# Kernel optimization log

Hardware: AMD Instinct MI355X
Metric: run time of the kernel (lower is better)

The kernel has to match this reference:

```python
import jax, jax.numpy as jnp
import numpy as np

B, S, D, M, E, K = 4, 1024, 2048, 512, 8, 2
AUX_W = 0.01


def setup_inputs() -> dict:
    key = jax.random.key(0)
    ks = jax.random.split(key, 9)
    n = lambda k, sh, fan: jax.random.normal(k, sh, jnp.float32) * (fan ** -0.5)
    return {
        "hidden_states": jax.random.normal(ks[0], (B, S, D), jnp.float32),
        "w_router": n(ks[1], (D, E), D),
        "wi0": n(ks[2], (E, D, M), D),
        "wi1": n(ks[3], (E, D, M), D),
        "wo": n(ks[4], (E, M, D), M),
        "sw_wi0": n(ks[5], (D, M), D),
        "sw_wi1": n(ks[6], (D, M), D),
        "sw_wo": n(ks[7], (M, D), M),
        "w_shared_gate": n(ks[8], (D, 1), D),
        "deterministic": 1,
    }


def reference(hidden_states, w_router, wi0, wi1, wo, sw_wi0, sw_wi1, sw_wo, w_shared_gate, deterministic):
    b, s, d = hidden_states.shape
    x = hidden_states.reshape(-1, d)  # [T, D]
    T = x.shape[0]

    # --- router: softmax over experts, top-k, renormalize top-k weights ---
    logits = (x @ w_router).astype(jnp.float32)           # [T, E]
    probs = jax.nn.softmax(logits, axis=-1)
    top_w, top_i = jax.lax.top_k(probs, K)                # [T, K]
    top_w = top_w / jnp.sum(top_w, axis=-1, keepdims=True)
    one_hot = jax.nn.one_hot(top_i, E, dtype=probs.dtype)  # [T, K, E]
    combine = jnp.einsum("tk,tke->te", top_w, one_hot)     # [T, E] sparse combine weights

    # --- load-balance aux loss (MaxText style) ---
    density = jnp.mean(jnp.sum(one_hot, axis=1), axis=0)    # fraction routed per expert
    density_proxy = jnp.mean(probs, axis=0)                 # mean router prob per expert
    load_balance_loss = jnp.mean(density * density_proxy) * (E * E) * AUX_W

    # --- routed experts: scan over experts, gated MLP, weighted combine ---
    def expert_step(acc, packed):
        wi0_e, wi1_e, wo_e, w_e = packed  # [D,M],[D,M],[M,D],[T]
        h = jax.nn.silu(x @ wi0_e) * (x @ wi1_e)            # [T, M]
        return acc + w_e[:, None] * (h @ wo_e), None

    routed, _ = jax.lax.scan(
        expert_step, jnp.zeros_like(x), (wi0, wi1, wo, combine.T)
    )

    # --- shared expert (gated MLP) + sigmoid shared gate ---
    hs = jax.nn.silu(x @ sw_wi0) * (x @ sw_wi1)
    shared = hs @ sw_wo                                     # [T, D]
    gate = jax.nn.sigmoid(x @ w_shared_gate)                # [T, 1]

    out = (routed + gate * shared).reshape(b, s, d)
    return out, load_balance_loss
```

## Files before the change

### kernel.cpp

```cpp
#include <hip/hip_runtime.h>
#include <hip/hip_bf16.h>
#include <math.h>

#define TT 4096
#define DD 2048
#define MM 512
#define EE 8

typedef __attribute__((ext_vector_type(8))) short short8;
typedef __attribute__((ext_vector_type(4))) float f32x4;

#define BARRIER() asm volatile("s_barrier" ::: "memory")

__device__ __forceinline__ unsigned short f2bf(float f) {
  union { float f; unsigned u; } v; v.f = f;
  unsigned u = v.u;
  unsigned r = u + 0x7FFFu + ((u >> 16) & 1u);
  return (unsigned short)(r >> 16);
}

__device__ __forceinline__ float bf2f(unsigned short u) {
  union { unsigned u; float f; } v; v.u = ((unsigned)u) << 16;
  return v.f;
}

__device__ __forceinline__ int imin(int a, int b) { return a < b ? a : b; }

__device__ __forceinline__ void gld16(const void* g, void* l) {
  __builtin_amdgcn_global_load_lds(
      (const __attribute__((address_space(1))) void*)g,
      (__attribute__((address_space(3))) void*)l, 16, 0, 0);
}

__global__ __launch_bounds__(256) void transpose_kernel(
    const float* __restrict__ wi0, const float* __restrict__ wi1,
    const float* __restrict__ wo, const float* __restrict__ swi0,
    const float* __restrict__ swi1, const float* __restrict__ swo,
    unsigned short* __restrict__ wi0T, unsigned short* __restrict__ wi1T,
    unsigned short* __restrict__ woT, unsigned short* __restrict__ swi0T,
    unsigned short* __restrict__ swi1T, unsigned short* __restrict__ swoT)
{
  int b = blockIdx.x;
  int tid = threadIdx.x;
  int slice = b >> 6, q = b & 63;
  const float* s; unsigned short* d;
  int R, C, tcb;
  if (slice < 8)       { s = wi0 + (size_t)slice * DD * MM;        d = wi0T + (size_t)slice * DD * MM;        R = DD; C = MM; tcb = 3; }
  else if (slice < 16) { s = wi1 + (size_t)(slice - 8) * DD * MM;  d = wi1T + (size_t)(slice - 8) * DD * MM;  R = DD; C = MM; tcb = 3; }
  else if (slice < 24) { s = wo + (size_t)(slice - 16) * MM * DD;  d = woT + (size_t)(slice - 16) * MM * DD;  R = MM; C = DD; tcb = 5; }
  else if (slice == 24){ s = swi0; d = swi0T; R = DD; C = MM; tcb = 3; }
  else if (slice == 25){ s = swi1; d = swi1T; R = DD; C = MM; tcb = 3; }
  else                 { s = swo;  d = swoT;  R = MM; C = DD; tcb = 5; }
  int ncmask = (1 << tcb) - 1;

  int wv = tid >> 6, lane = tid & 63;
  int t = q * 4 + wv;
  int c0 = (t & ncmask) * 64, r0 = (t >> tcb) * 64;
  int r8 = (lane >> 3) * 8;
  int c8 = (lane & 7) * 8;

  const float* sp = s + (size_t)(r0 + r8) * C + (c0 + c8);
  float4 v[8][2];
#pragma unroll
  for (int j = 0; j < 8; ++j) {
    v[j][0] = *(const float4*)&sp[(size_t)j * C];
    v[j][1] = *(const float4*)&sp[(size_t)j * C + 4];
  }
  __builtin_amdgcn_sched_barrier(0);
  unsigned short u[8][8];
#pragma unroll
  for (int j = 0; j < 8; ++j) {
    u[j][0] = f2bf(v[j][0].x); u[j][1] = f2bf(v[j][0].y);
    u[j][2] = f2bf(v[j][0].z); u[j][3] = f2bf(v[j][0].w);
    u[j][4] = f2bf(v[j][1].x); u[j][5] = f2bf(v[j][1].y);
    u[j][6] = f2bf(v[j][1].z); u[j][7] = f2bf(v[j][1].w);
  }
  unsigned short* dp = d + (size_t)(c0 + c8) * R + (r0 + r8);
#pragma unroll
  for (int c = 0; c < 8; ++c) {
    short8 o;
#pragma unroll
    for (int j = 0; j < 8; ++j) o[j] = (short)u[j][c];
    *(short8*)&dp[(size_t)c * R] = o;
  }
}

__global__ __launch_bounds__(256) void router_kernel(
    const float* __restrict__ x, const float* __restrict__ wr,
    const float* __restrict__ wg, unsigned short* __restrict__ xb,
    int* __restrict__ topk_i, float* __restrict__ topk_w,
    float* __restrict__ gate, int* __restrict__ cnt, float* __restrict__ proxy)
{
  __shared__ float s_proxy[EE];
  __shared__ int s_cnt[EE];
  int rb = blockIdx.x;
  int tid = threadIdx.x;
  if (tid < EE) { s_proxy[tid] = 0.f; s_cnt[tid] = 0; }
  __syncthreads();
  int wave = tid >> 6, lane = tid & 63;
  int t = rb * 4 + wave;
  const float* xr = x + (size_t)t * DD;
  unsigned short* xbr = xb + (size_t)t * DD;

  float xv[32], wgv[32];
#pragma unroll
  for (int i = 0; i < 32; ++i) xv[i] = xr[lane + i * 64];
#pragma unroll
  for (int i = 0; i < 32; ++i) wgv[i] = wg[lane + i * 64];
#pragma unroll
  for (int i = 0; i < 32; ++i) xbr[lane + i * 64] = f2bf(xv[i]);

  float p[EE];
#pragma unroll
  for (int e = 0; e < EE; ++e) p[e] = 0.f;
  float pg = 0.f;
  for (int i = 0; i < DD / 64; ++i) {
    int d = lane + i * 64;
    const float* w = wr + d * EE;
#pragma unroll
    for (int e = 0; e < EE; ++e) p[e] = fmaf(xv[i], w[e], p[e]);
    pg = fmaf(xv[i], wgv[i], pg);
  }
#pragma unroll
  for (int e = 0; e < EE; ++e) {
#pragma unroll
    for (int off = 32; off; off >>= 1) p[e] += __shfl_xor(p[e], off);
  }
#pragma unroll
  for (int off = 32; off; off >>= 1) pg += __shfl_xor(pg, off);

  if (lane == 0) {
    float mx = p[0];
#pragma unroll
    for (int e = 1; e < EE; ++e) mx = fmaxf(mx, p[e]);
    float pr[EE]; float s = 0.f;
#pragma unroll
    for (int e = 0; e < EE; ++e) { pr[e] = __expf(p[e] - mx); s += pr[e]; }
    float inv = 1.f / s;
#pragma unroll
    for (int e = 0; e < EE; ++e) pr[e] *= inv;
    int i0 = 0;
#pragma unroll
    for (int e = 1; e < EE; ++e) if (p[e] > p[i0]) i0 = e;
    int i1 = (i0 == 0) ? 1 : 0;
#pragma unroll
    for (int e = 0; e < EE; ++e) if (e != i0 && p[e] > p[i1]) i1 = e;
    float w0 = pr[i0], w1 = pr[i1], s2 = w0 + w1;
    topk_i[t * 2] = i0; topk_i[t * 2 + 1] = i1;
    topk_w[t * 2] = w0 / s2; topk_w[t * 2 + 1] = w1 / s2;
    gate[t] = 1.f / (1.f + __expf(-pg));
    atomicAdd(&s_cnt[i0], 1);
    atomicAdd(&s_cnt[i1], 1);
#pragma unroll
    for (int e = 0; e < EE; ++e) atomicAdd(&s_proxy[e], pr[e]);
  }
  __syncthreads();
  if (tid < EE) {
    atomicAdd(&cnt[tid], s_cnt[tid]);
    atomicAdd(&proxy[tid], s_proxy[tid]);
  }
}

__global__ void offsets_loss_kernel(const int* __restrict__ cnt, int* __restrict__ offs,
                                    const float* __restrict__ proxy, float* __restrict__ out_loss)
{
  if (threadIdx.x == 0 && blockIdx.x == 0) {
    int acc = 0; float l = 0.f;
    for (int e = 0; e < EE; ++e) {
      offs[e] = acc; acc += cnt[e];
      l += (float)cnt[e] * proxy[e];
    }
    out_loss[0] = l * (0.01f * (float)EE) / ((float)TT * (float)TT);
  }
}

__global__ void fill_kernel(const int* __restrict__ topk_i,
                            const int* __restrict__ offs, int* __restrict__ fillc,
                            int* __restrict__ btok, int* __restrict__ slotOf)
{
  int idx = blockIdx.x * blockDim.x + threadIdx.x;
  if (idx >= TT * 2) return;
  int e = topk_i[idx];
  int slot = atomicAdd(&fillc[e], 1);
  int p = offs[e] + slot;
  btok[p] = idx >> 1;
  slotOf[idx] = p;
}

__global__ __launch_bounds__(256) void gemm1_kernel(
    const unsigned short* __restrict__ xb,
    const unsigned short* __restrict__ wi0T, const unsigned short* __restrict__ wi1T,
    const unsigned short* __restrict__ swi0T, const unsigned short* __restrict__ swi1T,
    unsigned short* __restrict__ H, unsigned short* __restrict__ Hs,
    const int* __restrict__ btok, const int* __restrict__ cnt, const int* __restrict__ offs)
{
  __shared__ __align__(16) unsigned short lA0[128 * 64];
  __shared__ __align__(16) unsigned short lA1[128 * 64];
  __shared__ __align__(16) unsigned short lB0[128 * 64];
  __shared__ __align__(16) unsigned short lB1[128 * 64];
  int z = blockIdx.z;
  const unsigned short *w0, *w1;
  const int* tok = nullptr;
  unsigned short* Ho;
  int n;
  if (z < EE) {
    n = cnt[z];
    int rb = offs[z];
    tok = btok + rb;
    w0 = wi0T + (size_t)z * (DD * MM);
    w1 = wi1T + (size_t)z * (DD * MM);
    Ho = H + (size_t)rb * MM;
  } else { n = TT; w0 = swi0T; w1 = swi1T; Ho = Hs; }
  int row0 = blockIdx.y * 128;
  if (row0 >= n) return;
  int m0 = blockIdx.x * 64;
  int tid = threadIdx.x, lane = tid & 63, wv = tid >> 6;

  int lsub = lane >> 3;
  int chl = (lane & 7) ^ lsub;

  const unsigned short* gA[4];
  const unsigned short* gB[4];
#pragma unroll
  for (int c = 0; c < 4; ++c) {
    int row = c * 32 + wv * 8 + lsub;
    int tr;
    if (tok) tr = tok[imin(row0 + row, n - 1)];
    else     tr = row0 + row;
    gA[c] = xb + (size_t)tr * DD + chl * 8;
    int mat = row >> 6, col = row & 63;
    const unsigned short* wsel = mat ? w1 : w0;
    gB[c] = wsel + (size_t)(m0 + col) * DD + chl * 8;
  }

  int rw = (wv & 1) * 64;
  int cg = (wv >> 1) * 32;
  int fr = lane & 15;
  int grp = lane >> 4;
  int lr4 = (lane >> 4) * 4, lc = lane & 15;

  f32x4 acc[4][4];
  f32x4 zf = {0.f, 0.f, 0.f, 0.f};
#pragma unroll
  for (int i = 0; i < 4; ++i)
#pragma unroll
    for (int c = 0; c < 4; ++c) acc[i][c] = zf;

  auto stage = [&](int kk, unsigned short* la, unsigned short* lb) {
#pragma unroll
    for (int c = 0; c < 4; ++c) gld16(gA[c] + kk, la + c * 2048 + wv * 512);
#pragma unroll
    for (int c = 0; c < 4; ++c) gld16(gB[c] + kk, lb + c * 2048 + wv * 512);
  };
  auto compute = [&](const unsigned short* la, const unsigned short* lb) {
#pragma unroll
    for (int s = 0; s < 2; ++s) {
      int cq = s * 4 + grp;
      short8 af[4], bf[4];
#pragma unroll
      for (int i = 0; i < 4; ++i) {
        int row = rw + i * 16 + fr;
        af[i] = *(const short8*)&la[row * 64 + ((cq ^ (row & 7)) * 8)];
      }
#pragma unroll
      for (int c = 0; c < 4; ++c) {
        int rowb = (c >> 1) * 64 + cg + (c & 1) * 16 + fr;
        bf[c] = *(const short8*)&lb[rowb * 64 + ((cq ^ (rowb & 7)) * 8)];
      }
#pragma unroll
      for (int i = 0; i < 4; ++i)
#pragma unroll
        for (int c = 0; c < 4; ++c)
          acc[i][c] = __builtin_amdgcn_mfma_f32_16x16x32_bf16(af[i], bf[c], acc[i][c], 0, 0, 0);
    }
  };

  stage(0, lA0, lB0);
  stage(64, lA1, lB1);
  asm volatile("s_waitcnt vmcnt(8)" ::: "memory");
  BARRIER();

#pragma unroll 1
  for (int j = 0; j < DD / 128 - 1; ++j) {
    int k0 = j * 128;
    compute(lA0, lB0);
    BARRIER();
    stage(k0 + 128, lA0, lB0);
    asm volatile("s_waitcnt vmcnt(8)" ::: "memory");
    BARRIER();
    compute(lA1, lB1);
    BARRIER();
    stage(k0 + 192, lA1, lB1);
    asm volatile("s_waitcnt vmcnt(8)" ::: "memory");
    BARRIER();
  }
  compute(lA0, lB0);
  asm volatile("s_waitcnt vmcnt(0)" ::: "memory");
  BARRIER();
  compute(lA1, lB1);

#pragma unroll
  for (int i = 0; i < 4; ++i) {
#pragma unroll
    for (int c = 0; c < 2; ++c) {
#pragma unroll
      for (int rg = 0; rg < 4; ++rg) {
        int row = row0 + rw + i * 16 + lr4 + rg;
        if (row < n) {
          float a0 = acc[i][c][rg];
          float a1 = acc[i][c + 2][rg];
          float h = a0 / (1.f + __expf(-a0)) * a1;
          Ho[(size_t)row * MM + m0 + cg + c * 16 + lc] = f2bf(h);
        }
      }
    }
  }
}

__global__ __launch_bounds__(256) void gemm2_kernel(
    const unsigned short* __restrict__ H, const unsigned short* __restrict__ Hs,
    const unsigned short* __restrict__ woT, const unsigned short* __restrict__ swoT,
    unsigned short* __restrict__ Yr, unsigned short* __restrict__ Ys,
    const int* __restrict__ cnt, const int* __restrict__ offs)
{
  __shared__ __align__(16) unsigned short lA0[128 * 64];
  __shared__ __align__(16) unsigned short lA1[128 * 64];
  __shared__ __align__(16) unsigned short lB0[128 * 64];
  __shared__ __align__(16) unsigned short lB1[128 * 64];
  int z = blockIdx.z;
  int n, rb;
  const unsigned short *Hb, *wb;
  unsigned short* Yd;
  if (z < EE) { n = cnt[z]; rb = offs[z]; Hb = H + (size_t)rb * MM; wb = woT + (size_t)z * (DD * MM); Yd = Yr + (size_t)rb * DD; }
  else        { n = TT; rb = 0; Hb = Hs; wb = swoT; Yd = Ys; }
  int row0 = blockIdx.y * 128;
  if (row0 >= n) return;
  int d0 = blockIdx.x * 128;
  int tid = threadIdx.x, lane = tid & 63, wv = tid >> 6;

  int lsub = lane >> 3;
  int chl = (lane & 7) ^ lsub;

  const unsigned short* gA[4];
  const unsigned short* gB[4];
#pragma unroll
  for (int c = 0; c < 4; ++c) {
    int row = c * 32 + wv * 8 + lsub;
    int sr = imin(row0 + row, n - 1);
    gA[c] = Hb + (size_t)sr * MM + chl * 8;
    gB[c] = wb + (size_t)(d0 + row) * MM + chl * 8;
  }

  int rw = (wv & 1) * 64;
  int cw = (wv >> 1) * 64;
  int fr = lane & 15;
  int grp = lane >> 4;
  int lr4 = (lane >> 4) * 4, lc = lane & 15;

  f32x4 acc[4][4];
  f32x4 zf = {0.f, 0.f, 0.f, 0.f};
#pragma unroll
  for (int i = 0; i < 4; ++i)
#pragma unroll
    for (int c = 0; c < 4; ++c) acc[i][c] = zf;

  auto stage = [&](int kk, unsigned short* la, unsigned short* lb) {
#pragma unroll
    for (int c = 0; c < 4; ++c) gld16(gA[c] + kk, la + c * 2048 + wv * 512);
#pragma unroll
    for (int c = 0; c < 4; ++c) gld16(gB[c] + kk, lb + c * 2048 + wv * 512);
  };
  auto compute = [&](const unsigned short* la, const unsigned short* lb) {
#pragma unroll
    for (int s = 0; s < 2; ++s) {
      int cq = s * 4 + grp;
      short8 af[4], bf[4];
#pragma unroll
      for (int i = 0; i < 4; ++i) {
        int row = rw + i * 16 + fr;
        af[i] = *(const short8*)&la[row * 64 + ((cq ^ (row & 7)) * 8)];
      }
#pragma unroll
      for (int c = 0; c < 4; ++c) {
        int rowb = cw + c * 16 + fr;
        bf[c] = *(const short8*)&lb[rowb * 64 + ((cq ^ (rowb & 7)) * 8)];
      }
#pragma unroll
      for (int i = 0; i < 4; ++i)
#pragma unroll
        for (int c = 0; c < 4; ++c)
          acc[i][c] = __builtin_amdgcn_mfma_f32_16x16x32_bf16(af[i], bf[c], acc[i][c], 0, 0, 0);
    }
  };

  stage(0, lA0, lB0);
  stage(64, lA1, lB1);
  asm volatile("s_waitcnt vmcnt(8)" ::: "memory");
  BARRIER();

#pragma unroll 1
  for (int j = 0; j < MM / 128 - 1; ++j) {
    int k0 = j * 128;
    compute(lA0, lB0);
    BARRIER();
    stage(k0 + 128, lA0, lB0);
    asm volatile("s_waitcnt vmcnt(8)" ::: "memory");
    BARRIER();
    compute(lA1, lB1);
    BARRIER();
    stage(k0 + 192, lA1, lB1);
    asm volatile("s_waitcnt vmcnt(8)" ::: "memory");
    BARRIER();
  }
  compute(lA0, lB0);
  asm volatile("s_waitcnt vmcnt(0)" ::: "memory");
  BARRIER();
  compute(lA1, lB1);

#pragma unroll
  for (int i = 0; i < 4; ++i) {
#pragma unroll
    for (int c = 0; c < 4; ++c) {
#pragma unroll
      for (int rg = 0; rg < 4; ++rg) {
        int row = row0 + rw + i * 16 + lr4 + rg;
        if (row < n)
          Yd[(size_t)row * DD + d0 + cw + c * 16 + lc] = f2bf(acc[i][c][rg]);
      }
    }
  }
}

__global__ __launch_bounds__(256) void combine_kernel(
    const unsigned short* __restrict__ Yr, const unsigned short* __restrict__ Ys,
    const int* __restrict__ slotOf, const float* __restrict__ topk_w,
    const float* __restrict__ gate, float* __restrict__ out)
{
  int t = blockIdx.x;
  int d0 = threadIdx.x * 8;
  int p0 = slotOf[t * 2], p1 = slotOf[t * 2 + 1];
  float w0 = topk_w[t * 2], w1 = topk_w[t * 2 + 1], g = gate[t];
  short8 a = *(const short8*)&Yr[(size_t)p0 * DD + d0];
  short8 b = *(const short8*)&Yr[(size_t)p1 * DD + d0];
  short8 s = *(const short8*)&Ys[(size_t)t * DD + d0];
  float r[8];
#pragma unroll
  for (int j = 0; j < 8; ++j)
    r[j] = w0 * bf2f((unsigned short)a[j]) + w1 * bf2f((unsigned short)b[j])
         + g * bf2f((unsigned short)s[j]);
  float4 o0 = {r[0], r[1], r[2], r[3]};
  float4 o1 = {r[4], r[5], r[6], r[7]};
  float* op = out + (size_t)t * DD + d0;
  *(float4*)op = o0;
  *(float4*)(op + 4) = o1;
}

extern "C" void kernel_launch(void* const* d_in, const int* in_sizes, int n_in,
                              void* d_out, int out_size, void* d_ws, size_t ws_size,
                              hipStream_t stream) {
  const float* x    = (const float*)d_in[0];
  const float* wr   = (const float*)d_in[1];
  const float* wi0  = (const float*)d_in[2];
  const float* wi1  = (const float*)d_in[3];
  const float* wo   = (const float*)d_in[4];
  const float* swi0 = (const float*)d_in[5];
  const float* swi1 = (const float*)d_in[6];
  const float* swo  = (const float*)d_in[7];
  const float* wg   = (const float*)d_in[8];
  float* out = (float*)d_out;

  char* ws = (char*)d_ws;
  int*   cnt    = (int*)(ws + 0);
  int*   fillc  = (int*)(ws + 64);
  int*   offs   = (int*)(ws + 128);
  float* proxy  = (float*)(ws + 192);
  int*   topk_i = (int*)(ws + 1024);
  float* topk_w = (float*)(ws + 33792);
  int*   btok   = (int*)(ws + 66560);
  float* gate   = (float*)(ws + 132096);
  int*   slotOf = (int*)(ws + 148480);
  unsigned short* xb    = (unsigned short*)(ws + 1048576);
  unsigned short* H     = (unsigned short*)(ws + 17825792);
  unsigned short* Hs    = (unsigned short*)(ws + 26214400);
  unsigned short* wi0T  = (unsigned short*)(ws + 30408704);
  unsigned short* wi1T  = (unsigned short*)(ws + 47185920);
  unsigned short* woT   = (unsigned short*)(ws + 63963136);
  unsigned short* swi0T = (unsigned short*)(ws + 80740352);
  unsigned short* swi1T = (unsigned short*)(ws + 82837504);
  unsigned short* swoT  = (unsigned short*)(ws + 84934656);
  unsigned short* Ys = xb;
  unsigned short* Yr = wi0T;

  hipMemsetAsync(ws, 0, 256, stream);

  router_kernel<<<TT / 4, 256, 0, stream>>>(
      x, wr, wg, xb, topk_i, topk_w, gate, cnt, proxy);
  transpose_kernel<<<27 * 64, 256, 0, stream>>>(
      wi0, wi1, wo, swi0, swi1, swo, wi0T, wi1T, woT, swi0T, swi1T, swoT);
  offsets_loss_kernel<<<1, 64, 0, stream>>>(cnt, offs, proxy, out + (size_t)TT * DD);
  fill_kernel<<<(TT * 2) / 256, 256, 0, stream>>>(topk_i, offs, fillc, btok, slotOf);

  gemm1_kernel<<<dim3(MM / 64, 32, EE + 1), 256, 0, stream>>>(
      xb, wi0T, wi1T, swi0T, swi1T, H, Hs, btok, cnt, offs);
  gemm2_kernel<<<dim3(DD / 128, 32, EE + 1), 256, 0, stream>>>(
      H, Hs, woT, swoT, Yr, Ys, cnt, offs);
  combine_kernel<<<TT, 256, 0, stream>>>(Yr, Ys, slotOf, topk_w, gate, out);
}
```

Measured before the change: 226.5 us.

## Fuse transpose and router kernels; replace global atomics with partial-sum reductions

```diff
diff --git a/kernel.cpp b/kernel.cpp
--- a/kernel.cpp
+++ b/kernel.cpp
@@ -32,69 +32,70 @@
       (__attribute__((address_space(3))) void*)l, 16, 0, 0);
 }
 
-__global__ __launch_bounds__(256) void transpose_kernel(
+__global__ __launch_bounds__(256) void prep_kernel(
     const float* __restrict__ wi0, const float* __restrict__ wi1,
     const float* __restrict__ wo, const float* __restrict__ swi0,
     const float* __restrict__ swi1, const float* __restrict__ swo,
     unsigned short* __restrict__ wi0T, unsigned short* __restrict__ wi1T,
     unsigned short* __restrict__ woT, unsigned short* __restrict__ swi0T,
-    unsigned short* __restrict__ swi1T, unsigned short* __restrict__ swoT)
-{
-  int b = blockIdx.x;
-  int tid = threadIdx.x;
-  int slice = b >> 6, q = b & 63;
-  const float* s; unsigned short* d;
-  int R, C, tcb;
-  if (slice < 8)       { s = wi0 + (size_t)slice * DD * MM;        d = wi0T + (size_t)slice * DD * MM;        R = DD; C = MM; tcb = 3; }
-  else if (slice < 16) { s = wi1 + (size_t)(slice - 8) * DD * MM;  d = wi1T + (size_t)(slice - 8) * DD * MM;  R = DD; C = MM; tcb = 3; }
-  else if (slice < 24) { s = wo + (size_t)(slice - 16) * MM * DD;  d = woT + (size_t)(slice - 16) * MM * DD;  R = MM; C = DD; tcb = 5; }
-  else if (slice == 24){ s = swi0; d = swi0T; R = DD; C = MM; tcb = 3; }
-  else if (slice == 25){ s = swi1; d = swi1T; R = DD; C = MM; tcb = 3; }
-  else                 { s = swo;  d = swoT;  R = MM; C = DD; tcb = 5; }
-  int ncmask = (1 << tcb) - 1;
-
-  int wv = tid >> 6, lane = tid & 63;
-  int t = q * 4 + wv;
-  int c0 = (t & ncmask) * 64, r0 = (t >> tcb) * 64;
-  int r8 = (lane >> 3) * 8;
-  int c8 = (lane & 7) * 8;
-
-  const float* sp = s + (size_t)(r0 + r8) * C + (c0 + c8);
-  float4 v[8][2];
-#pragma unroll
-  for (int j = 0; j < 8; ++j) {
-    v[j][0] = *(const float4*)&sp[(size_t)j * C];
-    v[j][1] = *(const float4*)&sp[(size_t)j * C + 4];
-  }
-  __builtin_amdgcn_sched_barrier(0);
-  unsigned short u[8][8];
-#pragma unroll
-  for (int j = 0; j < 8; ++j) {
-    u[j][0] = f2bf(v[j][0].x); u[j][1] = f2bf(v[j][0].y);
-    u[j][2] = f2bf(v[j][0].z); u[j][3] = f2bf(v[j][0].w);
-    u[j][4] = f2bf(v[j][1].x); u[j][5] = f2bf(v[j][1].y);
-    u[j][6] = f2bf(v[j][1].z); u[j][7] = f2bf(v[j][1].w);
-  }
-  unsigned short* dp = d + (size_t)(c0 + c8) * R + (r0 + r8);
-#pragma unroll
-  for (int c = 0; c < 8; ++c) {
-    short8 o;
-#pragma unroll
-    for (int j = 0; j < 8; ++j) o[j] = (short)u[j][c];
-    *(short8*)&dp[(size_t)c * R] = o;
-  }
-}
-
-__global__ __launch_bounds__(256) void router_kernel(
+    unsigned short* __restrict__ swi1T, unsigned short* __restrict__ swoT,
     const float* __restrict__ x, const float* __restrict__ wr,
     const float* __restrict__ wg, unsigned short* __restrict__ xb,
     int* __restrict__ topk_i, float* __restrict__ topk_w,
-    float* __restrict__ gate, int* __restrict__ cnt, float* __restrict__ proxy)
+    float* __restrict__ gate, int* __restrict__ cnt_part,
+    float* __restrict__ proxy_part)
 {
   __shared__ float s_proxy[EE];
   __shared__ int s_cnt[EE];
-  int rb = blockIdx.x;
+  int b = blockIdx.x;
   int tid = threadIdx.x;
+
+  if (b < 27 * 64) {
+    int slice = b >> 6, q = b & 63;
+    const float* s; unsigned short* d;
+    int R, C, tcb;
+    if (slice < 8)       { s = wi0 + (size_t)slice * DD * MM;        d = wi0T + (size_t)slice * DD * MM;        R = DD; C = MM; tcb = 3; }
+    else if (slice < 16) { s = wi1 + (size_t)(slice - 8) * DD * MM;  d = wi1T + (size_t)(slice - 8) * DD * MM;  R = DD; C = MM; tcb = 3; }
+    else if (slice < 24) { s = wo + (size_t)(slice - 16) * MM * DD;  d = woT + (size_t)(slice - 16) * MM * DD;  R = MM; C = DD; tcb = 5; }
+    else if (slice == 24){ s = swi0; d = swi0T; R = DD; C = MM; tcb = 3; }
+    else if (slice == 25){ s = swi1; d = swi1T; R = DD; C = MM; tcb = 3; }
+    else                 { s = swo;  d = swoT;  R = MM; C = DD; tcb = 5; }
+    int ncmask = (1 << tcb) - 1;
+
+    int wv = tid >> 6, lane = tid & 63;
+    int t = q * 4 + wv;
+    int c0 = (t & ncmask) * 64, r0 = (t >> tcb) * 64;
+    int r8 = (lane >> 3) * 8;
+    int c8 = (lane & 7) * 8;
+
+    const float* sp = s + (size_t)(r0 + r8) * C + (c0 + c8);
+    float4 v[8][2];
+#pragma unroll
+    for (int j = 0; j < 8; ++j) {
+      v[j][0] = *(const float4*)&sp[(size_t)j * C];
+      v[j][1] = *(const float4*)&sp[(size_t)j * C + 4];
+    }
+    __builtin_amdgcn_sched_barrier(0);
+    unsigned short u[8][8];
+#pragma unroll
+    for (int j = 0; j < 8; ++j) {
+      u[j][0] = f2bf(v[j][0].x); u[j][1] = f2bf(v[j][0].y);
+      u[j][2] = f2bf(v[j][0].z); u[j][3] = f2bf(v[j][0].w);
+      u[j][4] = f2bf(v[j][1].x); u[j][5] = f2bf(v[j][1].y);
+      u[j][6] = f2bf(v[j][1].z); u[j][7] = f2bf(v[j][1].w);
+    }
+    unsigned short* dp = d + (size_t)(c0 + c8) * R + (r0 + r8);
+#pragma unroll
+    for (int c = 0; c < 8; ++c) {
+      short8 o;
+#pragma unroll
+      for (int j = 0; j < 8; ++j) o[j] = (short)u[j][c];
+      *(short8*)&dp[(size_t)c * R] = o;
+    }
+    return;
+  }
+
+  int rb = b - 27 * 64;
   if (tid < EE) { s_proxy[tid] = 0.f; s_cnt[tid] = 0; }
   __syncthreads();
   int wave = tid >> 6, lane = tid & 63;
@@ -156,33 +157,58 @@
   }
   __syncthreads();
   if (tid < EE) {
-    atomicAdd(&cnt[tid], s_cnt[tid]);
-    atomicAdd(&proxy[tid], s_proxy[tid]);
-  }
-}
-
-__global__ void offsets_loss_kernel(const int* __restrict__ cnt, int* __restrict__ offs,
-                                    const float* __restrict__ proxy, float* __restrict__ out_loss)
+    cnt_part[rb * EE + tid] = s_cnt[tid];
+    proxy_part[rb * EE + tid] = s_proxy[tid];
+  }
+}
+
+__global__ __launch_bounds__(256) void offsets_loss_kernel(
+    const int* __restrict__ cnt_part, const float* __restrict__ proxy_part,
+    int* __restrict__ cnt, int* __restrict__ offs, float* __restrict__ out_loss)
 {
-  if (threadIdx.x == 0 && blockIdx.x == 0) {
+  __shared__ int sc[256];
+  __shared__ float sp[256];
+  int tid = threadIdx.x;
+  int e = tid & 7, g = tid >> 3;
+  int ci = 0; float pi = 0.f;
+  for (int b = g; b < TT / 4; b += 32) {
+    ci += cnt_part[b * EE + e];
+    pi += proxy_part[b * EE + e];
+  }
+  sc[tid] = ci; sp[tid] = pi;
+  __syncthreads();
+  if (tid < EE) {
+    int c = 0; float p = 0.f;
+    for (int g2 = 0; g2 < 32; ++g2) { c += sc[g2 * 8 + tid]; p += sp[g2 * 8 + tid]; }
+    cnt[tid] = c;
+    sc[tid] = c; sp[tid] = p;
+  }
+  __syncthreads();
+  if (tid == 0) {
     int acc = 0; float l = 0.f;
-    for (int e = 0; e < EE; ++e) {
-      offs[e] = acc; acc += cnt[e];
-      l += (float)cnt[e] * proxy[e];
+    for (int e2 = 0; e2 < EE; ++e2) {
+      offs[e2] = acc; acc += sc[e2];
+      l += (float)sc[e2] * sp[e2];
     }
     out_loss[0] = l * (0.01f * (float)EE) / ((float)TT * (float)TT);
   }
 }
 
-__global__ void fill_kernel(const int* __restrict__ topk_i,
-                            const int* __restrict__ offs, int* __restrict__ fillc,
-                            int* __restrict__ btok, int* __restrict__ slotOf)
+__global__ __launch_bounds__(256) void fill_kernel(
+    const int* __restrict__ topk_i, const int* __restrict__ offs,
+    int* __restrict__ fillc, int* __restrict__ btok, int* __restrict__ slotOf)
 {
-  int idx = blockIdx.x * blockDim.x + threadIdx.x;
-  if (idx >= TT * 2) return;
+  __shared__ int lh[EE], gb[EE];
+  int tid = threadIdx.x;
+  int idx = blockIdx.x * 256 + tid;
+  if (tid < EE) lh[tid] = 0;
+  __syncthreads();
   int e = topk_i[idx];
-  int slot = atomicAdd(&fillc[e], 1);
-  int p = offs[e] + slot;
+  int r = atomicAdd(&lh[e], 1);
+  __syncthreads();
+  if (tid < EE) gb[tid] = atomicAdd(&fillc[tid], lh[tid]);
+  __syncthreads();
+  int p = offs[e] + gb[e] + r;
   btok[p] = idx >> 1;
   slotOf[idx] = p;
 }
@@ -473,12 +499,13 @@
   int*   cnt    = (int*)(ws + 0);
   int*   fillc  = (int*)(ws + 64);
   int*   offs   = (int*)(ws + 128);
-  float* proxy  = (float*)(ws + 192);
   int*   topk_i = (int*)(ws + 1024);
   float* topk_w = (float*)(ws + 33792);
   int*   btok   = (int*)(ws + 66560);
   float* gate   = (float*)(ws + 132096);
   int*   slotOf = (int*)(ws + 148480);
+  int*   cnt_part   = (int*)(ws + 262144);
+  float* proxy_part = (float*)(ws + 294912);
   unsigned short* xb    = (unsigned short*)(ws + 1048576);
   unsigned short* H     = (unsigned short*)(ws + 17825792);
   unsigned short* Hs    = (unsigned short*)(ws + 26214400);
@@ -493,11 +520,11 @@
 
   hipMemsetAsync(ws, 0, 256, stream);
 
-  router_kernel<<<TT / 4, 256, 0, stream>>>(
-      x, wr, wg, xb, topk_i, topk_w, gate, cnt, proxy);
-  transpose_kernel<<<27 * 64, 256, 0, stream>>>(
-      wi0, wi1, wo, swi0, swi1, swo, wi0T, wi1T, woT, swi0T, swi1T, swoT);
-  offsets_loss_kernel<<<1, 64, 0, stream>>>(cnt, offs, proxy, out + (size_t)TT * DD);
+  prep_kernel<<<27 * 64 + TT / 4, 256, 0, stream>>>(
+      wi0, wi1, wo, swi0, swi1, swo, wi0T, wi1T, woT, swi0T, swi1T, swoT,
+      x, wr, wg, xb, topk_i, topk_w, gate, cnt_part, proxy_part);
+  offsets_loss_kernel<<<1, 256, 0, stream>>>(
+      cnt_part, proxy_part, cnt, offs, out + (size_t)TT * DD);
   fill_kernel<<<(TT * 2) / 256, 256, 0, stream>>>(topk_i, offs, fillc, btok, slotOf);
 
   gemm1_kernel<<<dim3(MM / 64, 32, EE + 1), 256, 0, stream>>>(
```

Result: faster. 197.3 us (-12.9%).
